# Performance work log

Hardware: AMD Instinct MI355X
Metric: run time of the kernel (lower is better)

Reference implementation:

```python
import jax, jax.numpy as jnp
import numpy as np

N, E, B, DIM, NF, EF, HID = 50000, 100000, 2000, 64, 14, 4, 128


def setup_inputs() -> dict:
    key = jax.random.key(0)
    ks = jax.random.split(key, 30)
    rn = lambda k, shape, scale: jax.random.normal(k, shape, jnp.float32) * scale
    inp = {}
    inp["x"] = rn(ks[0], (N, NF), 1.0)
    inp["edge_attr"] = jax.random.uniform(ks[1], (E, EF), jnp.float32)
    inp["edge_index"] = jax.random.randint(ks[2], (2, E), 0, N)
    # equal-size graphs: 25 nodes per graph, sorted segment ids
    inp["batch"] = (jnp.arange(N, dtype=jnp.int32) // (N // B)).astype(jnp.int32)
    inp["lin0_w"] = rn(ks[3], (DIM, NF), (1.0 / NF) ** 0.5)
    inp["lin0_b"] = jnp.zeros((DIM,), jnp.float32)
    inp["mlp_w1"] = rn(ks[4], (HID, EF), (1.0 / EF) ** 0.5)
    inp["mlp_b1"] = jnp.zeros((HID,), jnp.float32)
    inp["mlp_w2"] = rn(ks[5], (DIM * DIM, HID), (1.0 / HID) ** 0.5)
    inp["mlp_b2"] = jnp.zeros((DIM * DIM,), jnp.float32)
    inp["root"] = rn(ks[6], (DIM, DIM), (1.0 / DIM) ** 0.5)
    inp["conv_b"] = jnp.zeros((DIM,), jnp.float32)
    inp["gru_wih"] = rn(ks[7], (3 * DIM, DIM), (1.0 / DIM) ** 0.5)
    inp["gru_whh"] = rn(ks[8], (3 * DIM, DIM), (1.0 / DIM) ** 0.5)
    inp["gru_bih"] = jnp.zeros((3 * DIM,), jnp.float32)
    inp["gru_bhh"] = jnp.zeros((3 * DIM,), jnp.float32)
    inp["lstm_wih"] = rn(ks[9], (4 * DIM, 2 * DIM), (1.0 / (2 * DIM)) ** 0.5)
    inp["lstm_whh"] = rn(ks[10], (4 * DIM, DIM), (1.0 / DIM) ** 0.5)
    inp["lstm_bih"] = jnp.zeros((4 * DIM,), jnp.float32)
    inp["lstm_bhh"] = jnp.zeros((4 * DIM,), jnp.float32)
    inp["lin1_w"] = rn(ks[11], (DIM, 2 * DIM), (1.0 / (2 * DIM)) ** 0.5)
    inp["lin1_b"] = jnp.zeros((DIM,), jnp.float32)
    inp["lin2_w"] = rn(ks[12], (1, DIM), (1.0 / DIM) ** 0.5)
    inp["lin2_b"] = jnp.zeros((1,), jnp.float32)
    return inp


def _forward(x, edge_attr, edge_index, batch, lin0_w, lin0_b, mlp_w1, mlp_b1,
             mlp_w2, mlp_b2, root, conv_b, gru_wih, gru_whh, gru_bih, gru_bhh,
             lstm_wih, lstm_whh, lstm_bih, lstm_bhh, lin1_w, lin1_b, lin2_w, lin2_b):
    src, dst = edge_index[0], edge_index[1]
    n = x.shape[0]
    # edge MLP -> per-edge weight matrices [E, DIM, DIM]
    h_e = jax.nn.relu(edge_attr @ mlp_w1.T + mlp_b1)
    W_e = (h_e @ mlp_w2.T + mlp_b2).reshape(-1, DIM, DIM)
    deg = jnp.clip(jax.ops.segment_sum(jnp.ones_like(dst, jnp.float32), dst, n), 1.0)

    out = jax.nn.relu(x @ lin0_w.T + lin0_b)
    h = out  # GRU hidden (seq_len=1, 1 layer)
    for _ in range(3):
        msg = jnp.einsum('ei,eio->eo', out[src], W_e)  # per-edge matmul
        agg = jax.ops.segment_sum(msg, dst, n) / deg[:, None]  # scatter-mean
        m = jax.nn.relu(agg + out @ root + conv_b)  # NNConv: aggr + root + bias
        # GRU step
        gi = m @ gru_wih.T + gru_bih
        gh = h @ gru_whh.T + gru_bhh
        i_r, i_z, i_n = jnp.split(gi, 3, axis=-1)
        h_r, h_z, h_n = jnp.split(gh, 3, axis=-1)
        r = jax.nn.sigmoid(i_r + h_r)
        z = jax.nn.sigmoid(i_z + h_z)
        ng = jnp.tanh(i_n + r * h_n)
        h = (1.0 - z) * ng + z * h
        out = h

    # Set2Set pooling, 3 processing steps
    b = B
    qh = jnp.zeros((b, DIM), out.dtype)
    qc = jnp.zeros((b, DIM), out.dtype)
    q_star = jnp.zeros((b, 2 * DIM), out.dtype)
    for _ in range(3):
        gates = q_star @ lstm_wih.T + lstm_bih + qh @ lstm_whh.T + lstm_bhh
        gi_, gf_, gg_, go_ = jnp.split(gates, 4, axis=-1)
        qc = jax.nn.sigmoid(gf_) * qc + jax.nn.sigmoid(gi_) * jnp.tanh(gg_)
        qh = jax.nn.sigmoid(go_) * jnp.tanh(qc)
        q = qh
        e = jnp.sum(out * q[batch], axis=-1)  # [N]
        e_max = jax.ops.segment_max(e, batch, b)
        a = jnp.exp(e - e_max[batch])
        denom = jax.ops.segment_sum(a, batch, b)
        a = a / denom[batch]
        r_read = jax.ops.segment_sum(a[:, None] * out, batch, b)
        q_star = jnp.concatenate([q, r_read], axis=-1)

    y = jax.nn.relu(q_star @ lin1_w.T + lin1_b)
    y = y @ lin2_w.T + lin2_b
    return y.reshape(-1)


def reference(x, edge_attr, edge_index, batch, lin0_w, lin0_b, mlp_w1, mlp_b1,
              mlp_w2, mlp_b2, root, conv_b, gru_wih, gru_whh, gru_bih, gru_bhh,
              lstm_wih, lstm_whh, lstm_bih, lstm_bhh, lin1_w, lin1_b, lin2_w, lin2_b):
    return _forward(x, edge_attr, edge_index, batch, lin0_w, lin0_b, mlp_w1, mlp_b1,
                    mlp_w2, mlp_b2, root, conv_b, gru_wih, gru_whh, gru_bih, gru_bhh,
                    lstm_wih, lstm_whh, lstm_bih, lstm_bhh, lin1_w, lin1_b, lin2_w, lin2_b)
```

## Files before the change

### kernel.cpp

```cpp
#include <hip/hip_runtime.h>
#include <hip/hip_bf16.h>

#define NN 50000
#define EE 100000
#define BB 2000
#define DIM 64
#define NF 14
#define EF 4
#define HID 128
#define EPAD 100096

typedef __attribute__((ext_vector_type(8))) _Float16 half8;
typedef __attribute__((ext_vector_type(4))) _Float16 half4;
typedef __attribute__((ext_vector_type(4))) float floatx4;

__global__ void transpose_kernel(const float* __restrict__ lih, const float* __restrict__ lhh,
                                 const float* __restrict__ l1,
                                 float* __restrict__ lihT, float* __restrict__ lhhT,
                                 float* __restrict__ l1T) {
    int t = blockIdx.x * 256 + threadIdx.x;
    if (t < 256 * 128) { int j = t / 128, k = t % 128; lihT[k * 256 + j] = lih[t]; }
    if (t < 256 * 64) { int j = t / 64, k = t % 64; lhhT[k * 256 + j] = lhh[t]; }
    if (t < 64 * 128) { int d = t / 128, k = t % 128; l1T[k * 64 + d] = l1[t]; }
}

__global__ void prep_gru_kernel(const float* __restrict__ root, const float* __restrict__ b2,
                                const float* __restrict__ wih, const float* __restrict__ whh,
                                const float* __restrict__ bih, const float* __restrict__ bhh,
                                _Float16* __restrict__ W1h, _Float16* __restrict__ W2h,
                                float* __restrict__ fbias) {
    int t = blockIdx.x * 256 + threadIdx.x;
    if (t < 64 * 128) {
        int n = t >> 7, k = t & 127;
        W1h[t] = (_Float16)(k < 64 ? root[k * 64 + n] : b2[(size_t)(k - 64) * 64 + n]);
    }
    if (t < 256 * 128) {
        int n2 = t >> 7, k = t & 127;
        int g = n2 >> 6, j = n2 & 63;
        float v;
        if (g == 0)      v = (k < 64) ? wih[j * 64 + k]         : whh[j * 64 + (k - 64)];
        else if (g == 1) v = (k < 64) ? wih[(64 + j) * 64 + k]  : whh[(64 + j) * 64 + (k - 64)];
        else if (g == 2) v = (k < 64) ? wih[(128 + j) * 64 + k] : 0.f;
        else             v = (k < 64) ? 0.f                     : whh[(128 + j) * 64 + (k - 64)];
        W2h[t] = (_Float16)v;
    }
    if (t < 256) {
        int g = t >> 6, j = t & 63;
        float v = (g == 0) ? bih[j] + bhh[j]
                : (g == 1) ? bih[64 + j] + bhh[64 + j]
                : (g == 2) ? bih[128 + j] : bhh[128 + j];
        fbias[t] = v;
    }
}

__global__ void lin0_kernel(const float* __restrict__ x, const float* __restrict__ w,
                            const float* __restrict__ b, float* __restrict__ hv) {
    int t = blockIdx.x * 256 + threadIdx.x;
    if (t >= NN * 64) return;
    int n = t >> 6, d = t & 63;
    float acc = b[d];
    #pragma unroll
    for (int f = 0; f < NF; f++) acc += x[n * NF + f] * w[d * NF + f];
    hv[t] = fmaxf(acc, 0.f);
}

__global__ void deg_kernel(const int* __restrict__ ei, float* __restrict__ deg) {
    int e = blockIdx.x * 256 + threadIdx.x;
    if (e < EE) atomicAdd(&deg[ei[EE + e]], 1.0f);
}

__global__ void he16_kernel(const float* __restrict__ ea, const float* __restrict__ w1,
                            const float* __restrict__ b1, _Float16* __restrict__ he) {
    int t = blockIdx.x * 256 + threadIdx.x;
    if (t >= EPAD * 128) return;
    int el = t >> 7, h = t & 127;
    float acc = 0.f;
    if (el < EE) {
        const float4 a = *(const float4*)(ea + (size_t)el * 4);
        const float4 w = *(const float4*)(w1 + h * 4);
        acc = fmaxf(b1[h] + a.x * w.x + a.y * w.y + a.z * w.z + a.w * w.w, 0.f);
    }
    he[t] = (_Float16)acc;
}

__global__ void w2rt_kernel(const float* __restrict__ w2, _Float16* __restrict__ W2rT) {
    int t = blockIdx.x * 256 + threadIdx.x;
    if (t >= 64 * 8192) return;
    int o = t >> 13, k = t & 8191, i = k >> 7, h = k & 127;
    W2rT[(size_t)o * 8192 + k] = (_Float16)w2[(size_t)(i * 64 + o) * 128 + h];
}

__global__ __launch_bounds__(256, 2) void msg_gemm_kernel(
    const float* __restrict__ hv, const _Float16* __restrict__ he16,
    const _Float16* __restrict__ W2rT, const int* __restrict__ ei,
    float* __restrict__ agg, float* __restrict__ xsum) {
    __shared__ _Float16 sB[2][16 * 64 * 8];
    __shared__ _Float16 sXs[256 * 68];
    __shared__ int sDst[256];
    const int t = threadIdx.x;
    const int eb = blockIdx.x * 256;
    const int lane = t & 63;
    const int w = t >> 6;
    const int col = lane & 15;
    const int quad = lane >> 4;

    if (t < 256) {
        int e = eb + t;
        sDst[t] = (e < EE) ? ei[EE + e] : 0;
    }
    #pragma unroll 4
    for (int rep = 0; rep < 16; rep++) {
        int idx = rep * 256 + t;
        int el = idx >> 4, d4 = idx & 15;
        int e = eb + el;
        float4 v = {0.f, 0.f, 0.f, 0.f};
        if (e < EE) {
            int src = ei[e];
            v = *(const float4*)(hv + (size_t)src * 64 + d4 * 4);
        }
        half4 h4 = {(_Float16)v.x, (_Float16)v.y, (_Float16)v.z, (_Float16)v.w};
        *(half4*)&sXs[el * 68 + d4 * 4] = h4;
    }

    half8 heReg[4][4];
    #pragma unroll
    for (int mt = 0; mt < 4; mt++) {
        int row = eb + w * 64 + mt * 16 + col;
        #pragma unroll
        for (int p = 0; p < 4; p++)
            heReg[mt][p] = *(const half8*)(he16 + (size_t)row * 128 + p * 32 + quad * 8);
    }

    floatx4 Cacc[4][4];
    #pragma unroll
    for (int mt = 0; mt < 4; mt++)
        #pragma unroll
        for (int nt = 0; nt < 4; nt++)
            Cacc[mt][nt] = (floatx4){0.f, 0.f, 0.f, 0.f};

    const size_t gbase = (size_t)(w * 16 + col) * 8192 + quad * 8;
    half8 pre[4];
    {
        #pragma unroll
        for (int rep = 0; rep < 4; rep++)
            pre[rep] = *(const half8*)(W2rT + gbase + 0 * 128 + rep * 32);
        #pragma unroll
        for (int rep = 0; rep < 4; rep++)
            *(half8*)&sB[0][((w * 4 + rep) * 64 + lane) * 8] = pre[rep];
    }
    __syncthreads();

    #pragma unroll 1
    for (int i = 0; i < 64; i++) {
        int buf = i & 1;
        if (i < 63) {
            #pragma unroll
            for (int rep = 0; rep < 4; rep++)
                pre[rep] = *(const half8*)(W2rT + gbase + (size_t)(i + 1) * 128 + rep * 32);
        }
        _Float16 xsx[4];
        #pragma unroll
        for (int mt = 0; mt < 4; mt++)
            xsx[mt] = sXs[(w * 64 + mt * 16 + col) * 68 + i];
        #pragma unroll
        for (int ks = 0; ks < 4; ks++) {
            half8 bfr[4];
            #pragma unroll
            for (int nt = 0; nt < 4; nt++)
                bfr[nt] = *(const half8*)&sB[buf][((nt * 4 + ks) * 64 + lane) * 8];
            #pragma unroll
            for (int mt = 0; mt < 4; mt++) {
                half8 afr = heReg[mt][ks] * xsx[mt];
                #pragma unroll
                for (int nt = 0; nt < 4; nt++)
                    Cacc[mt][nt] = __builtin_amdgcn_mfma_f32_16x16x32_f16(afr, bfr[nt], Cacc[mt][nt], 0, 0, 0);
            }
        }
        if (i < 63) {
            #pragma unroll
            for (int rep = 0; rep < 4; rep++)
                *(half8*)&sB[buf ^ 1][((w * 4 + rep) * 64 + lane) * 8] = pre[rep];
        }
        __syncthreads();
    }

    #pragma unroll
    for (int mt = 0; mt < 4; mt++) {
        #pragma unroll
        for (int r = 0; r < 4; r++) {
            int el = w * 64 + mt * 16 + quad * 4 + r;
            if (eb + el < EE) {
                float* ap = agg + (size_t)sDst[el] * 64 + col;
                #pragma unroll
                for (int nt = 0; nt < 4; nt++)
                    atomicAdd(ap + nt * 16, Cacc[mt][nt][r]);
            }
        }
    }
    #pragma unroll 4
    for (int rep = 0; rep < 64; rep++) {
        int idx = rep * 256 + t;
        int el = idx >> 6, d = idx & 63;
        if (eb + el < EE)
            atomicAdd(&xsum[(size_t)sDst[el] * 64 + d], (float)sXs[el * 68 + d]);
    }
}

__global__ __launch_bounds__(256, 2) void node_fused_kernel(
    const float* __restrict__ hv_in, float* __restrict__ agg,
    float* __restrict__ xsum, const float* __restrict__ deg,
    const _Float16* __restrict__ W1h, const _Float16* __restrict__ W2h,
    const float* __restrict__ fbias, const float* __restrict__ cb,
    float* __restrict__ hv_out) {
    __shared__ _Float16 sA1[64 * 136];
    __shared__ _Float16 sA2[64 * 136];
    __shared__ float sH[64 * 68];
    __shared__ float sAgg[64 * 68];
    const int t = threadIdx.x;
    const int nb = blockIdx.x * 64;
    const int n = t >> 2, part = t & 3;
    {
        int gn = nb + n;
        bool valid = gn < NN;
        float inv = 1.f;
        if (valid) inv = 1.f / fmaxf(deg[gn], 1.f);
        #pragma unroll
        for (int c4 = 0; c4 < 4; c4++) {
            int d0 = part * 16 + c4 * 4;
            float4 hvv = {0.f, 0.f, 0.f, 0.f}, agv = {0.f, 0.f, 0.f, 0.f}, xsv = {0.f, 0.f, 0.f, 0.f};
            if (valid) {
                hvv = *(const float4*)(hv_in + (size_t)gn * 64 + d0);
                agv = *(const float4*)(agg + (size_t)gn * 64 + d0);
                xsv = *(const float4*)(xsum + (size_t)gn * 64 + d0);
            }
            agv.x *= inv; agv.y *= inv; agv.z *= inv; agv.w *= inv;
            xsv.x *= inv; xsv.y *= inv; xsv.z *= inv; xsv.w *= inv;
            half4 hvh = {(_Float16)hvv.x, (_Float16)hvv.y, (_Float16)hvv.z, (_Float16)hvv.w};
            half4 xsh = {(_Float16)xsv.x, (_Float16)xsv.y, (_Float16)xsv.z, (_Float16)xsv.w};
            *(half4*)&sA1[n * 136 + d0] = hvh;
            *(half4*)&sA1[n * 136 + 64 + d0] = xsh;
            *(half4*)&sA2[n * 136 + 64 + d0] = hvh;
            *(float4*)&sH[n * 68 + d0] = hvv;
            *(float4*)&sAgg[n * 68 + d0] = agv;
        }
        if (valid) {
            float4 z = {0.f, 0.f, 0.f, 0.f};
            #pragma unroll
            for (int c4 = 0; c4 < 4; c4++) {
                int d0 = part * 16 + c4 * 4;
                *(float4*)(agg + (size_t)gn * 64 + d0) = z;
                *(float4*)(xsum + (size_t)gn * 64 + d0) = z;
            }
        }
    }
    __syncthreads();

    const int lane = t & 63, w = t >> 6;
    const int col = lane & 15, quad = lane >> 4;

    floatx4 C1[4];
    #pragma unroll
    for (int nt = 0; nt < 4; nt++) {
        float b = cb[nt * 16 + col];
        C1[nt] = (floatx4){b, b, b, b};
    }
    #pragma unroll
    for (int ks = 0; ks < 4; ks++) {
        half8 a = *(const half8*)&sA1[(w * 16 + col) * 136 + ks * 32 + quad * 8];
        #pragma unroll
        for (int nt = 0; nt < 4; nt++) {
            half8 bfr = *(const half8*)(W1h + (size_t)(nt * 16 + col) * 128 + ks * 32 + quad * 8);
            C1[nt] = __builtin_amdgcn_mfma_f32_16x16x32_f16(a, bfr, C1[nt], 0, 0, 0);
        }
    }
    #pragma unroll
    for (int nt = 0; nt < 4; nt++) {
        #pragma unroll
        for (int r = 0; r < 4; r++) {
            int node = w * 16 + quad * 4 + r;
            int j = nt * 16 + col;
            float m = fmaxf(C1[nt][r] + sAgg[node * 68 + j], 0.f);
            sA2[node * 136 + j] = (_Float16)m;
        }
    }
    __syncthreads();

    floatx4 C2[16];
    #pragma unroll
    for (int nt2 = 0; nt2 < 16; nt2++) {
        float b = fbias[nt2 * 16 + col];
        C2[nt2] = (floatx4){b, b, b, b};
    }
    #pragma unroll
    for (int ks = 0; ks < 4; ks++) {
        half8 a = *(const half8*)&sA2[(w * 16 + col) * 136 + ks * 32 + quad * 8];
        #pragma unroll
        for (int nt2 = 0; nt2 < 16; nt2++) {
            half8 bfr = *(const half8*)(W2h + (size_t)(nt2 * 16 + col) * 128 + ks * 32 + quad * 8);
            C2[nt2] = __builtin_amdgcn_mfma_f32_16x16x32_f16(a, bfr, C2[nt2], 0, 0, 0);
        }
    }
    float hnew[4][4];
    #pragma unroll
    for (int r = 0; r < 4; r++) {
        int node = w * 16 + quad * 4 + r;
        #pragma unroll
        for (int jt = 0; jt < 4; jt++) {
            int j = jt * 16 + col;
            float rr = 1.f / (1.f + expf(-C2[jt][r]));
            float zz = 1.f / (1.f + expf(-C2[4 + jt][r]));
            float ng = tanhf(C2[8 + jt][r] + rr * C2[12 + jt][r]);
            float hold = sH[node * 68 + j];
            hnew[r][jt] = (1.f - zz) * ng + zz * hold;
        }
    }
    __syncthreads();
    #pragma unroll
    for (int r = 0; r < 4; r++) {
        int node = w * 16 + quad * 4 + r;
        #pragma unroll
        for (int jt = 0; jt < 4; jt++)
            sH[node * 68 + jt * 16 + col] = hnew[r][jt];
    }
    __syncthreads();
    {
        int gn = nb + n;
        if (gn < NN) {
            #pragma unroll
            for (int c4 = 0; c4 < 4; c4++) {
                int d0 = part * 16 + c4 * 4;
                *(float4*)(hv_out + (size_t)gn * 64 + d0) = *(const float4*)&sH[n * 68 + d0];
            }
        }
    }
}

__global__ __launch_bounds__(256) void set2set_kernel(
    const float* __restrict__ hv,
    const float* __restrict__ lihT, const float* __restrict__ lhhT,
    const float* __restrict__ l_bih, const float* __restrict__ l_bhh,
    const float* __restrict__ lin1T, const float* __restrict__ lin1_b,
    const float* __restrict__ lin2_w, const float* __restrict__ lin2_b,
    float* __restrict__ out) {
    __shared__ float outS[25 * 65];
    __shared__ float qs[128], qh[64], qc[64], gat[256], ew[32], aw[32], red[64];
    int g = blockIdx.x;
    int t = threadIdx.x;
    for (int p = t; p < 25 * 64; p += 256) {
        int j = p >> 6, i = p & 63;
        outS[j * 65 + i] = hv[(size_t)(g * 25 + j) * 64 + i];
    }
    if (t < 128) qs[t] = 0.f;
    if (t < 64) { qh[t] = 0.f; qc[t] = 0.f; }
    __syncthreads();
    for (int it = 0; it < 3; it++) {
        float acc = l_bih[t] + l_bhh[t];
        for (int k = 0; k < 128; k++) acc += qs[k] * lihT[k * 256 + t];
        for (int k = 0; k < 64; k++) acc += qh[k] * lhhT[k * 256 + t];
        gat[t] = acc;
        __syncthreads();
        if (t < 64) {
            float ig = 1.f / (1.f + expf(-gat[t]));
            float fg = 1.f / (1.f + expf(-gat[64 + t]));
            float gg = tanhf(gat[128 + t]);
            float og = 1.f / (1.f + expf(-gat[192 + t]));
            float c = fg * qc[t] + ig * gg;
            qc[t] = c;
            qh[t] = og * tanhf(c);
        }
        __syncthreads();
        if (t < 25) {
            float e = 0.f;
            for (int i = 0; i < 64; i++) e += outS[t * 65 + i] * qh[i];
            ew[t] = e;
        }
        __syncthreads();
        if (t == 0) {
            float mx = ew[0];
            for (int j = 1; j < 25; j++) mx = fmaxf(mx, ew[j]);
            float s = 0.f;
            for (int j = 0; j < 25; j++) { float a = expf(ew[j] - mx); aw[j] = a; s += a; }
            float inv = 1.f / s;
            for (int j = 0; j < 25; j++) aw[j] *= inv;
        }
        __syncthreads();
        if (t < 64) {
            float r = 0.f;
            for (int j = 0; j < 25; j++) r += aw[j] * outS[j * 65 + t];
            qs[t] = qh[t];
            qs[64 + t] = r;
        }
        __syncthreads();
    }
    if (t < 64) {
        float y1 = lin1_b[t];
        for (int k = 0; k < 128; k++) y1 += qs[k] * lin1T[k * 64 + t];
        y1 = fmaxf(y1, 0.f);
        red[t] = y1 * lin2_w[t];
    }
    __syncthreads();
    if (t == 0) {
        float y = lin2_b[0];
        for (int i = 0; i < 64; i++) y += red[i];
        out[g] = y;
    }
}

extern "C" void kernel_launch(void* const* d_in, const int* in_sizes, int n_in,
                              void* d_out, int out_size, void* d_ws, size_t ws_size,
                              hipStream_t stream) {
    const float* x        = (const float*)d_in[0];
    const float* ea       = (const float*)d_in[1];
    const int*   ei       = (const int*)  d_in[2];
    const float* lin0_w   = (const float*)d_in[4];
    const float* lin0_b   = (const float*)d_in[5];
    const float* mlp_w1   = (const float*)d_in[6];
    const float* mlp_b1   = (const float*)d_in[7];
    const float* mlp_w2   = (const float*)d_in[8];
    const float* mlp_b2   = (const float*)d_in[9];
    const float* root     = (const float*)d_in[10];
    const float* conv_b   = (const float*)d_in[11];
    const float* gru_wih  = (const float*)d_in[12];
    const float* gru_whh  = (const float*)d_in[13];
    const float* gru_bih  = (const float*)d_in[14];
    const float* gru_bhh  = (const float*)d_in[15];
    const float* lstm_wih = (const float*)d_in[16];
    const float* lstm_whh = (const float*)d_in[17];
    const float* lstm_bih = (const float*)d_in[18];
    const float* lstm_bhh = (const float*)d_in[19];
    const float* lin1_w   = (const float*)d_in[20];
    const float* lin1_b   = (const float*)d_in[21];
    const float* lin2_w   = (const float*)d_in[22];
    const float* lin2_b   = (const float*)d_in[23];
    float* out = (float*)d_out;

    char* base = (char*)d_ws;
    size_t off = 0;
    auto carve = [&](size_t bytes) -> void* {
        void* r = base + off;
        off = (off + bytes + 255) & ~(size_t)255;
        return r;
    };
    float* hv   = (float*)carve((size_t)NN * 64 * 4);
    float* agg  = (float*)carve((size_t)NN * 64 * 4);
    float* xsum = (float*)carve((size_t)NN * 64 * 4);
    float* deg  = (float*)carve((size_t)NN * 4);
    float* lihT = (float*)carve(128 * 256 * 4);
    float* lhhT = (float*)carve(64 * 256 * 4);
    float* l1T  = (float*)carve(128 * 64 * 4);
    float* fbias = (float*)carve(256 * 4);
    _Float16* he16 = (_Float16*)carve((size_t)EPAD * 128 * 2);
    _Float16* W2rT = (_Float16*)carve((size_t)64 * 8192 * 2);
    _Float16* W1h  = (_Float16*)carve((size_t)64 * 128 * 2);
    _Float16* W2h  = (_Float16*)carve((size_t)256 * 128 * 2);

    hipMemsetAsync(deg, 0, (size_t)NN * 4, stream);
    hipMemsetAsync(agg, 0, (size_t)NN * 64 * 4 * 2, stream);
    transpose_kernel<<<128, 256, 0, stream>>>(lstm_wih, lstm_whh, lin1_w, lihT, lhhT, l1T);
    prep_gru_kernel<<<128, 256, 0, stream>>>(root, mlp_b2, gru_wih, gru_whh, gru_bih, gru_bhh,
                                             W1h, W2h, fbias);
    lin0_kernel<<<(NN * 64 + 255) / 256, 256, 0, stream>>>(x, lin0_w, lin0_b, hv);
    deg_kernel<<<(EE + 255) / 256, 256, 0, stream>>>(ei, deg);
    he16_kernel<<<(EPAD * 128 + 255) / 256, 256, 0, stream>>>(ea, mlp_w1, mlp_b1, he16);
    w2rt_kernel<<<(64 * 8192 + 255) / 256, 256, 0, stream>>>(mlp_w2, W2rT);

    for (int it = 0; it < 3; it++) {
        msg_gemm_kernel<<<EPAD / 256, 256, 0, stream>>>(hv, he16, W2rT, ei, agg, xsum);
        node_fused_kernel<<<(NN + 63) / 64, 256, 0, stream>>>(hv, agg, xsum, deg,
                                                              W1h, W2h, fbias, conv_b, hv);
    }

    set2set_kernel<<<BB, 256, 0, stream>>>(hv, lihT, lhhT, lstm_bih, lstm_bhh,
                                           l1T, lin1_b, lin2_w, lin2_b, out);
}
```

Baseline: 763.8 us.

## Fuse prep kernels, split message GEMM over K halves, use fast transcendentals

Merges the six setup kernels into one launch with vectorized per-thread work, and folds the deg memset into the agg/xsum memset because deg is carved right after them. It also splits each msg_gemm edge tile across two blocks, each covering half of the 64 input dimensions, doubling the grid from 391 blocks to raise occupancy on the many CUs. Both halves add partial results into agg with atomics, which adds atomic traffic. Finally it swaps expf, tanhf and divisions for fast exp/rcp intrinsics in the GRU and Set2Set, trading some accuracy.

Result: slower. 812.5 us (+6.4%).

```diff
diff --git a/kernel.cpp b/kernel.cpp
--- a/kernel.cpp
+++ b/kernel.cpp
@@ -14,22 +14,78 @@
 typedef __attribute__((ext_vector_type(4))) _Float16 half4;
 typedef __attribute__((ext_vector_type(4))) float floatx4;
 
-__global__ void transpose_kernel(const float* __restrict__ lih, const float* __restrict__ lhh,
-                                 const float* __restrict__ l1,
-                                 float* __restrict__ lihT, float* __restrict__ lhhT,
-                                 float* __restrict__ l1T) {
+__device__ __forceinline__ float rcp_fast(float x) { return __builtin_amdgcn_rcpf(x); }
+__device__ __forceinline__ float sig_fast(float x) { return rcp_fast(1.f + __expf(-x)); }
+__device__ __forceinline__ float tanh_fast(float x) {
+    float e = __expf(2.f * x);
+    return 1.f - 2.f * rcp_fast(e + 1.f);
+}
+
+__global__ void prep_fused_kernel(
+    const float* __restrict__ x, const float* __restrict__ lin0_w,
+    const float* __restrict__ lin0_b, float* __restrict__ hv,
+    const float* __restrict__ ea, const float* __restrict__ w1,
+    const float* __restrict__ b1, _Float16* __restrict__ he,
+    const int* __restrict__ ei, float* __restrict__ deg,
+    const float* __restrict__ w2, _Float16* __restrict__ W2rT,
+    const float* __restrict__ lih, const float* __restrict__ lhh,
+    const float* __restrict__ l1, float* __restrict__ lihT,
+    float* __restrict__ lhhT, float* __restrict__ l1T,
+    const float* __restrict__ root, const float* __restrict__ b2,
+    const float* __restrict__ gwih, const float* __restrict__ gwhh,
+    const float* __restrict__ gbih, const float* __restrict__ gbhh,
+    _Float16* __restrict__ W1h, _Float16* __restrict__ W2h,
+    float* __restrict__ fbias) {
     int t = blockIdx.x * 256 + threadIdx.x;
+
+    {
+        int el = t >> 4, hc = t & 15;
+        if (el < EPAD) {
+            half8 o8 = {0, 0, 0, 0, 0, 0, 0, 0};
+            if (el < EE) {
+                const float4 a = *(const float4*)(ea + (size_t)el * 4);
+                #pragma unroll
+                for (int j = 0; j < 8; j++) {
+                    int h = hc * 8 + j;
+                    const float4 w = *(const float4*)(w1 + h * 4);
+                    float acc = fmaxf(b1[h] + a.x * w.x + a.y * w.y + a.z * w.z + a.w * w.w, 0.f);
+                    o8[j] = (_Float16)acc;
+                }
+                if (hc == 0) atomicAdd(&deg[ei[EE + el]], 1.0f);
+            }
+            *(half8*)(he + (size_t)el * 128 + hc * 8) = o8;
+        }
+    }
+    if (t < NN * 8) {
+        int n = t >> 3, dc = t & 7;
+        float xv[NF];
+        #pragma unroll
+        for (int f = 0; f < NF; f++) xv[f] = x[(size_t)n * NF + f];
+        float o[8];
+        #pragma unroll
+        for (int j = 0; j < 8; j++) {
+            int d = dc * 8 + j;
+            float acc = lin0_b[d];
+            #pragma unroll
+            for (int f = 0; f < NF; f++) acc += xv[f] * lin0_w[d * NF + f];
+            o[j] = fmaxf(acc, 0.f);
+        }
+        *(float4*)(hv + (size_t)n * 64 + dc * 8)     = make_float4(o[0], o[1], o[2], o[3]);
+        *(float4*)(hv + (size_t)n * 64 + dc * 8 + 4) = make_float4(o[4], o[5], o[6], o[7]);
+    }
+    if (t < 64 * 1024) {
+        int o = t >> 10, kc = t & 1023;
+        int k0 = kc * 8, i = k0 >> 7, h0 = k0 & 127;
+        const float* src = w2 + (size_t)(i * 64 + o) * 128 + h0;
+        const float4 a = *(const float4*)src;
+        const float4 b = *(const float4*)(src + 4);
+        half8 r = {(_Float16)a.x, (_Float16)a.y, (_Float16)a.z, (_Float16)a.w,
+                   (_Float16)b.x, (_Float16)b.y, (_Float16)b.z, (_Float16)b.w};
+        *(half8*)(W2rT + (size_t)o * 8192 + k0) = r;
+    }
     if (t < 256 * 128) { int j = t / 128, k = t % 128; lihT[k * 256 + j] = lih[t]; }
     if (t < 256 * 64) { int j = t / 64, k = t % 64; lhhT[k * 256 + j] = lhh[t]; }
     if (t < 64 * 128) { int d = t / 128, k = t % 128; l1T[k * 64 + d] = l1[t]; }
-}
-
-__global__ void prep_gru_kernel(const float* __restrict__ root, const float* __restrict__ b2,
-                                const float* __restrict__ wih, const float* __restrict__ whh,
-                                const float* __restrict__ bih, const float* __restrict__ bhh,
-                                _Float16* __restrict__ W1h, _Float16* __restrict__ W2h,
-                                float* __restrict__ fbias) {
-    int t = blockIdx.x * 256 + threadIdx.x;
     if (t < 64 * 128) {
         int n = t >> 7, k = t & 127;
         W1h[t] = (_Float16)(k < 64 ? root[k * 64 + n] : b2[(size_t)(k - 64) * 64 + n]);
@@ -38,56 +94,19 @@
         int n2 = t >> 7, k = t & 127;
         int g = n2 >> 6, j = n2 & 63;
         float v;
-        if (g == 0)      v = (k < 64) ? wih[j * 64 + k]         : whh[j * 64 + (k - 64)];
-        else if (g == 1) v = (k < 64) ? wih[(64 + j) * 64 + k]  : whh[(64 + j) * 64 + (k - 64)];
-        else if (g == 2) v = (k < 64) ? wih[(128 + j) * 64 + k] : 0.f;
-        else             v = (k < 64) ? 0.f                     : whh[(128 + j) * 64 + (k - 64)];
+        if (g == 0)      v = (k < 64) ? gwih[j * 64 + k]         : gwhh[j * 64 + (k - 64)];
+        else if (g == 1) v = (k < 64) ? gwih[(64 + j) * 64 + k]  : gwhh[(64 + j) * 64 + (k - 64)];
+        else if (g == 2) v = (k < 64) ? gwih[(128 + j) * 64 + k] : 0.f;
+        else             v = (k < 64) ? 0.f                      : gwhh[(128 + j) * 64 + (k - 64)];
         W2h[t] = (_Float16)v;
     }
     if (t < 256) {
         int g = t >> 6, j = t & 63;
-        float v = (g == 0) ? bih[j] + bhh[j]
-                : (g == 1) ? bih[64 + j] + bhh[64 + j]
-                : (g == 2) ? bih[128 + j] : bhh[128 + j];
+        float v = (g == 0) ? gbih[j] + gbhh[j]
+                : (g == 1) ? gbih[64 + j] + gbhh[64 + j]
+                : (g == 2) ? gbih[128 + j] : gbhh[128 + j];
         fbias[t] = v;
     }
-}
-
-__global__ void lin0_kernel(const float* __restrict__ x, const float* __restrict__ w,
-                            const float* __restrict__ b, float* __restrict__ hv) {
-    int t = blockIdx.x * 256 + threadIdx.x;
-    if (t >= NN * 64) return;
-    int n = t >> 6, d = t & 63;
-    float acc = b[d];
-    #pragma unroll
-    for (int f = 0; f < NF; f++) acc += x[n * NF + f] * w[d * NF + f];
-    hv[t] = fmaxf(acc, 0.f);
-}
-
-__global__ void deg_kernel(const int* __restrict__ ei, float* __restrict__ deg) {
-    int e = blockIdx.x * 256 + threadIdx.x;
-    if (e < EE) atomicAdd(&deg[ei[EE + e]], 1.0f);
-}
-
-__global__ void he16_kernel(const float* __restrict__ ea, const float* __restrict__ w1,
-                            const float* __restrict__ b1, _Float16* __restrict__ he) {
-    int t = blockIdx.x * 256 + threadIdx.x;
-    if (t >= EPAD * 128) return;
-    int el = t >> 7, h = t & 127;
-    float acc = 0.f;
-    if (el < EE) {
-        const float4 a = *(const float4*)(ea + (size_t)el * 4);
-        const float4 w = *(const float4*)(w1 + h * 4);
-        acc = fmaxf(b1[h] + a.x * w.x + a.y * w.y + a.z * w.z + a.w * w.w, 0.f);
-    }
-    he[t] = (_Float16)acc;
-}
-
-__global__ void w2rt_kernel(const float* __restrict__ w2, _Float16* __restrict__ W2rT) {
-    int t = blockIdx.x * 256 + threadIdx.x;
-    if (t >= 64 * 8192) return;
-    int o = t >> 13, k = t & 8191, i = k >> 7, h = k & 127;
-    W2rT[(size_t)o * 8192 + k] = (_Float16)w2[(size_t)(i * 64 + o) * 128 + h];
 }
 
 __global__ __launch_bounds__(256, 2) void msg_gemm_kernel(
@@ -98,7 +117,10 @@
     __shared__ _Float16 sXs[256 * 68];
     __shared__ int sDst[256];
     const int t = threadIdx.x;
-    const int eb = blockIdx.x * 256;
+    const int tile = blockIdx.x >> 1;
+    const int ki = blockIdx.x & 1;
+    const int eb = tile * 256;
+    const int base = ki * 32;
     const int lane = t & 63;
     const int w = t >> 6;
     const int col = lane & 15;
@@ -108,18 +130,34 @@
         int e = eb + t;
         sDst[t] = (e < EE) ? ei[EE + e] : 0;
     }
-    #pragma unroll 4
-    for (int rep = 0; rep < 16; rep++) {
-        int idx = rep * 256 + t;
-        int el = idx >> 4, d4 = idx & 15;
-        int e = eb + el;
-        float4 v = {0.f, 0.f, 0.f, 0.f};
-        if (e < EE) {
-            int src = ei[e];
-            v = *(const float4*)(hv + (size_t)src * 64 + d4 * 4);
-        }
-        half4 h4 = {(_Float16)v.x, (_Float16)v.y, (_Float16)v.z, (_Float16)v.w};
-        *(half4*)&sXs[el * 68 + d4 * 4] = h4;
+    if (ki == 0) {
+        #pragma unroll 4
+        for (int rep = 0; rep < 16; rep++) {
+            int idx = rep * 256 + t;
+            int el = idx >> 4, d4 = idx & 15;
+            int e = eb + el;
+            float4 v = {0.f, 0.f, 0.f, 0.f};
+            if (e < EE) {
+                int src = ei[e];
+                v = *(const float4*)(hv + (size_t)src * 64 + d4 * 4);
+            }
+            half4 h4 = {(_Float16)v.x, (_Float16)v.y, (_Float16)v.z, (_Float16)v.w};
+            *(half4*)&sXs[el * 68 + d4 * 4] = h4;
+        }
+    } else {
+        #pragma unroll 4
+        for (int rep = 0; rep < 8; rep++) {
+            int idx = rep * 256 + t;
+            int el = idx >> 3, d4 = 8 + (idx & 7);
+            int e = eb + el;
+            float4 v = {0.f, 0.f, 0.f, 0.f};
+            if (e < EE) {
+                int src = ei[e];
+                v = *(const float4*)(hv + (size_t)src * 64 + d4 * 4);
+            }
+            half4 h4 = {(_Float16)v.x, (_Float16)v.y, (_Float16)v.z, (_Float16)v.w};
+            *(half4*)&sXs[el * 68 + d4 * 4] = h4;
+        }
     }
 
     half8 heReg[4][4];
@@ -143,7 +181,7 @@
     {
         #pragma unroll
         for (int rep = 0; rep < 4; rep++)
-            pre[rep] = *(const half8*)(W2rT + gbase + 0 * 128 + rep * 32);
+            pre[rep] = *(const half8*)(W2rT + gbase + (size_t)base * 128 + rep * 32);
         #pragma unroll
         for (int rep = 0; rep < 4; rep++)
             *(half8*)&sB[0][((w * 4 + rep) * 64 + lane) * 8] = pre[rep];
@@ -151,17 +189,17 @@
     __syncthreads();
 
     #pragma unroll 1
-    for (int i = 0; i < 64; i++) {
-        int buf = i & 1;
-        if (i < 63) {
+    for (int ii = 0; ii < 32; ii++) {
+        int buf = ii & 1;
+        if (ii < 31) {
             #pragma unroll
             for (int rep = 0; rep < 4; rep++)
-                pre[rep] = *(const half8*)(W2rT + gbase + (size_t)(i + 1) * 128 + rep * 32);
+                pre[rep] = *(const half8*)(W2rT + gbase + (size_t)(base + ii + 1) * 128 + rep * 32);
         }
         _Float16 xsx[4];
         #pragma unroll
         for (int mt = 0; mt < 4; mt++)
-            xsx[mt] = sXs[(w * 64 + mt * 16 + col) * 68 + i];
+            xsx[mt] = sXs[(w * 64 + mt * 16 + col) * 68 + base + ii];
         #pragma unroll
         for (int ks = 0; ks < 4; ks++) {
             half8 bfr[4];
@@ -176,7 +214,7 @@
                     Cacc[mt][nt] = __builtin_amdgcn_mfma_f32_16x16x32_f16(afr, bfr[nt], Cacc[mt][nt], 0, 0, 0);
             }
         }
-        if (i < 63) {
+        if (ii < 31) {
             #pragma unroll
             for (int rep = 0; rep < 4; rep++)
                 *(half8*)&sB[buf ^ 1][((w * 4 + rep) * 64 + lane) * 8] = pre[rep];
@@ -197,12 +235,14 @@
             }
         }
     }
-    #pragma unroll 4
-    for (int rep = 0; rep < 64; rep++) {
-        int idx = rep * 256 + t;
-        int el = idx >> 6, d = idx & 63;
-        if (eb + el < EE)
-            atomicAdd(&xsum[(size_t)sDst[el] * 64 + d], (float)sXs[el * 68 + d]);
+    if (ki == 0) {
+        #pragma unroll 4
+        for (int rep = 0; rep < 64; rep++) {
+            int idx = rep * 256 + t;
+            int el = idx >> 6, d = idx & 63;
+            if (eb + el < EE)
+                atomicAdd(&xsum[(size_t)sDst[el] * 64 + d], (float)sXs[el * 68 + d]);
+        }
     }
 }
 
@@ -307,9 +347,9 @@
         #pragma unroll
         for (int jt = 0; jt < 4; jt++) {
             int j = jt * 16 + col;
-            float rr = 1.f / (1.f + expf(-C2[jt][r]));
-            float zz = 1.f / (1.f + expf(-C2[4 + jt][r]));
-            float ng = tanhf(C2[8 + jt][r] + rr * C2[12 + jt][r]);
+            float rr = sig_fast(C2[jt][r]);
+            float zz = sig_fast(C2[4 + jt][r]);
+            float ng = tanh_fast(C2[8 + jt][r] + rr * C2[12 + jt][r]);
             float hold = sH[node * 68 + j];
             hnew[r][jt] = (1.f - zz) * ng + zz * hold;
         }
@@ -360,13 +400,13 @@
         gat[t] = acc;
         __syncthreads();
         if (t < 64) {
-            float ig = 1.f / (1.f + expf(-gat[t]));
-            float fg = 1.f / (1.f + expf(-gat[64 + t]));
-            float gg = tanhf(gat[128 + t]);
-            float og = 1.f / (1.f + expf(-gat[192 + t]));
+            float ig = sig_fast(gat[t]);
+            float fg = sig_fast(gat[64 + t]);
+            float gg = tanh_fast(gat[128 + t]);
+            float og = sig_fast(gat[192 + t]);
             float c = fg * qc[t] + ig * gg;
             qc[t] = c;
-            qh[t] = og * tanhf(c);
+            qh[t] = og * tanh_fast(c);
         }
         __syncthreads();
         if (t < 25) {
@@ -379,8 +419,8 @@
             float mx = ew[0];
             for (int j = 1; j < 25; j++) mx = fmaxf(mx, ew[j]);
             float s = 0.f;
-            for (int j = 0; j < 25; j++) { float a = expf(ew[j] - mx); aw[j] = a; s += a; }
-            float inv = 1.f / s;
+            for (int j = 0; j < 25; j++) { float a = __expf(ew[j] - mx); aw[j] = a; s += a; }
+            float inv = rcp_fast(s);
             for (int j = 0; j < 25; j++) aw[j] *= inv;
         }
         __syncthreads();
@@ -454,18 +494,17 @@
     _Float16* W1h  = (_Float16*)carve((size_t)64 * 128 * 2);
     _Float16* W2h  = (_Float16*)carve((size_t)256 * 128 * 2);
 
-    hipMemsetAsync(deg, 0, (size_t)NN * 4, stream);
-    hipMemsetAsync(agg, 0, (size_t)NN * 64 * 4 * 2, stream);
-    transpose_kernel<<<128, 256, 0, stream>>>(lstm_wih, lstm_whh, lin1_w, lihT, lhhT, l1T);
-    prep_gru_kernel<<<128, 256, 0, stream>>>(root, mlp_b2, gru_wih, gru_whh, gru_bih, gru_bhh,
-                                             W1h, W2h, fbias);
-    lin0_kernel<<<(NN * 64 + 255) / 256, 256, 0, stream>>>(x, lin0_w, lin0_b, hv);
-    deg_kernel<<<(EE + 255) / 256, 256, 0, stream>>>(ei, deg);
-    he16_kernel<<<(EPAD * 128 + 255) / 256, 256, 0, stream>>>(ea, mlp_w1, mlp_b1, he16);
-    w2rt_kernel<<<(64 * 8192 + 255) / 256, 256, 0, stream>>>(mlp_w2, W2rT);
+    hipMemsetAsync(agg, 0, (size_t)NN * 64 * 4 * 2 + (size_t)NN * 4, stream);
+    prep_fused_kernel<<<EPAD * 16 / 256, 256, 0, stream>>>(
+        x, lin0_w, lin0_b, hv,
+        ea, mlp_w1, mlp_b1, he16, ei, deg,
+        mlp_w2, W2rT,
+        lstm_wih, lstm_whh, lin1_w, lihT, lhhT, l1T,
+        root, mlp_b2, gru_wih, gru_whh, gru_bih, gru_bhh,
+        W1h, W2h, fbias);
 
     for (int it = 0; it < 3; it++) {
-        msg_gemm_kernel<<<EPAD / 256, 256, 0, stream>>>(hv, he16, W2rT, ei, agg, xsum);
+        msg_gemm_kernel<<<(EPAD / 256) * 2, 256, 0, stream>>>(hv, he16, W2rT, ei, agg, xsum);
         node_fused_kernel<<<(NN + 63) / 64, 256, 0, stream>>>(hv, agg, xsum, deg,
                                                               W1h, W2h, fbias, conv_b, hv);
     }
```
